# Optimization experiments

Measured on AMD Instinct MI355X. Metric: run time of the kernel, lower is better.

The kernel has to match this reference:

```python
import jax, jax.numpy as jnp
import numpy as np

N_HEAD = 16
N_EMBD = 1024
HEAD_DIM = N_EMBD // N_HEAD


def setup_inputs() -> dict:
    key = jax.random.key(0)
    k1, k2, k3 = jax.random.split(key, 3)
    B, T, C = 2, 2048, N_EMBD
    x = jax.random.normal(k1, (B, T, C), dtype=jnp.float32)
    # nn.Linear weights: (out_features, in_features)
    W_attn = jax.random.normal(k2, (3 * C, C), dtype=jnp.float32) * 0.02
    W_proj = jax.random.normal(k3, (C, C), dtype=jnp.float32) * 0.02
    return {"x": x, "W_attn": W_attn, "W_proj": W_proj}


def reference(x, W_attn, W_proj):
    B, T, C = x.shape
    h, hd = N_HEAD, HEAD_DIM
    # c_attn: x @ W^T, then split into q, k, v
    qkv = jnp.einsum('btc,dc->btd', x, W_attn)  # [B, T, 3C]
    q, k, v = jnp.split(qkv, 3, axis=-1)
    # [B, T, C] -> [B, h, T, hd]
    q = q.reshape(B, T, h, hd).transpose(0, 2, 1, 3)
    k = k.reshape(B, T, h, hd).transpose(0, 2, 1, 3)
    v = v.reshape(B, T, h, hd).transpose(0, 2, 1, 3)
    # NOTE: no 1/sqrt(hd) scaling in the original module
    logits = jnp.einsum('bhnk,bhmk->bhnm', q, k)  # [B, h, T, T]
    causal = jnp.tril(jnp.ones((T, T), dtype=bool))  # [T, T]
    logits = jnp.where(causal[None, None, :, :], logits, -jnp.inf)
    weights = jax.nn.softmax(logits, axis=-1)
    O = jnp.einsum('bhnm,bhmv->bhnv', weights, v)  # [B, h, T, hd]
    # Original: einsum('bhnv,hdv->bnd', O, c_proj.weight) with weight viewed as (h, d, v)
    Wp = W_proj.reshape(h, C, hd)
    Y = jnp.einsum('bhnv,hdv->bnd', O, Wp)  # [B, T, C]
    return Y
```

## Files before the change

### kernel.cpp

```cpp
#include <hip/hip_runtime.h>
#include <stdint.h>
#include <math.h>

#define B_    2
#define T_    2048
#define C_    1024
#define H_    16
#define D_    64
#define MTOT  4096
#define NQKV  3072
#define KDIM  1024

#define LOG2E 1.4426950408889634f

typedef short short8 __attribute__((ext_vector_type(8)));
typedef float f32x4  __attribute__((ext_vector_type(4)));

__device__ __forceinline__ uint16_t f2b(float f) {
    union { float f; uint32_t u; } x; x.f = f;
    uint32_t u = x.u;
    return (uint16_t)((u + 0x7FFFu + ((u >> 16) & 1u)) >> 16);
}
__device__ __forceinline__ uint32_t packb2(float a, float b) {
    union { float f; uint32_t u; } x, y; x.f = a; y.f = b;
    return __builtin_amdgcn_perm(y.u + 0x8000u, x.u + 0x8000u, 0x07060302u);
}
__device__ __forceinline__ uint32_t packb2_rne(float a, float b) {
    return (uint32_t)f2b(a) | ((uint32_t)f2b(b) << 16);
}
__device__ __forceinline__ float fexp2(float x) {
#if __has_builtin(__builtin_amdgcn_exp2f)
    return __builtin_amdgcn_exp2f(x);
#else
    return exp2f(x);
#endif
}

__global__ __launch_bounds__(256) void cast_all(const float* __restrict__ x,
                                                const float* __restrict__ wa,
                                                uint16_t* __restrict__ xb,
                                                uint16_t* __restrict__ wab,
                                                int n4x, int n4w) {
    int i = blockIdx.x * blockDim.x + threadIdx.x;
    const float* src; uint16_t* dst; int j;
    if (i < n4x) { src = x; dst = xb; j = i; }
    else { j = i - n4x; if (j >= n4w) return; src = wa; dst = wab; }
    float4 v = ((const float4*)src)[j];
    ushort4 o;
    o.x = f2b(v.x); o.y = f2b(v.y); o.z = f2b(v.z); o.w = f2b(v.w);
    ((ushort4*)dst)[j] = o;
}

__global__ __launch_bounds__(256) void cast_wp(const float* __restrict__ wp,
                                               uint16_t* __restrict__ wt) {
    int i = blockIdx.x * blockDim.x + threadIdx.x;
    int j4 = (i & 255) * 4;
    int d  = i >> 8;
    int h = j4 >> 6, v = j4 & 63;
    float4 val = *(const float4*)(wp + h * 65536 + d * 64 + v);
    ushort4 o;
    o.x = f2b(val.x); o.y = f2b(val.y); o.z = f2b(val.z); o.w = f2b(val.w);
    *(ushort4*)(wt + d * 1024 + j4) = o;
}

__global__ __launch_bounds__(256, 3) void gemm_qkv(const uint16_t* __restrict__ A,
                                                   const uint16_t* __restrict__ Bw,
                                                   uint16_t* __restrict__ qkvb) {
    __shared__ __align__(16) uint16_t As[128 * 64];
    __shared__ __align__(16) uint16_t Bs[128 * 64];

    int tid = threadIdx.x;
    int w = tid >> 6, lane = tid & 63;
    int qd = lane >> 4, ln = lane & 15;
    int lnx = ln & 7;
    int rowBase = blockIdx.y * 128;
    int colBase = blockIdx.x * 128;
    int mw = (w >> 1) * 64, nw = (w & 1) * 64;

    int srow = tid >> 3;
    int pchunk = tid & 7;
    int gchunk = pchunk ^ (srow & 7);

    const uint16_t* ga = A  + (size_t)(rowBase + srow) * KDIM + gchunk * 8;
    const uint16_t* gb = Bw + (size_t)(colBase + srow) * KDIM + gchunk * 8;
    uint16_t* la = &As[srow * 64 + pchunk * 8];
    uint16_t* lb = &Bs[srow * 64 + pchunk * 8];

    short8 pa[4], pb[4];
#pragma unroll
    for (int m = 0; m < 4; m++) {
        pa[m] = *(const short8*)(ga + (size_t)m * 32 * KDIM);
        pb[m] = *(const short8*)(gb + (size_t)m * 32 * KDIM);
    }

    f32x4 acc[4][4] = {};
    for (int s = 0; s < 16; s++) {
#pragma unroll
        for (int m = 0; m < 4; m++) {
            *(short8*)(la + m * 32 * 64) = pa[m];
            *(short8*)(lb + m * 32 * 64) = pb[m];
        }
        __syncthreads();
        if (s < 15) {
            int k0 = (s + 1) * 64;
#pragma unroll
            for (int m = 0; m < 4; m++) {
                pa[m] = *(const short8*)(ga + k0 + (size_t)m * 32 * KDIM);
                pb[m] = *(const short8*)(gb + k0 + (size_t)m * 32 * KDIM);
            }
        }
#pragma unroll
        for (int ks = 0; ks < 2; ks++) {
            int p = (ks * 4 + qd) ^ lnx;
            short8 a[4], b[4];
#pragma unroll
            for (int i = 0; i < 4; i++) {
                a[i] = *(const short8*)&As[(mw + i * 16 + ln) * 64 + p * 8];
                b[i] = *(const short8*)&Bs[(nw + i * 16 + ln) * 64 + p * 8];
            }
#pragma unroll
            for (int i = 0; i < 4; i++)
#pragma unroll
                for (int j = 0; j < 4; j++)
                    acc[i][j] = __builtin_amdgcn_mfma_f32_16x16x32_bf16(a[i], b[j], acc[i][j], 0, 0, 0);
        }
        __syncthreads();
    }

#pragma unroll
    for (int i = 0; i < 4; i++) {
#pragma unroll
        for (int j = 0; j < 4; j++) {
            int gcol = colBase + nw + j * 16 + ln;
            int which = gcol >> 10;
            int rem = gcol & 1023;
            int h = rem >> 6, d = rem & 63;
            float sc = (which == 0) ? LOG2E : 1.0f;
#pragma unroll
            for (int r = 0; r < 4; r++) {
                int grow = rowBase + mw + i * 16 + qd * 4 + r;
                int bb = grow >> 11, t = grow & 2047;
                uint16_t val = f2b(acc[i][j][r] * sc);
                if (which == 2) {
                    qkvb[(size_t)2 * 4194304 + (((size_t)(bb * H_ + h) * D_) + d) * T_ + t] = val;
                } else {
                    qkvb[(size_t)which * 4194304 + (((size_t)(bb * H_ + h) * T_) + t) * D_ + d] = val;
                }
            }
        }
    }
}

__global__ __launch_bounds__(256) void attn(const uint16_t* __restrict__ qkvb,
                                            uint16_t* __restrict__ oc) {
    union ShU {
        uint16_t Pl[4][64][72];
        f32x4 X[2][17][64];
    };
    __shared__ __align__(16) ShU sh;

    int tid = threadIdx.x;
    int w = tid >> 6, lane = tid & 63;
    int qd = lane >> 4, ln = lane & 15;
    int bid = blockIdx.x;
    int pr = bid >> 5;
    int bh = bid & 31;

    const uint16_t* Q  = qkvb + (size_t)bh * T_ * D_;
    const uint16_t* K  = Q + 4194304;
    const uint16_t* Vt = qkvb + (size_t)2 * 4194304 + (size_t)bh * D_ * T_;

    for (int phase = 0; phase < 2; phase++) {
        int qt = phase == 0 ? (31 - pr) : pr;
        int qbase = qt * 64;
        int ntiles = qt + 1;

        short8 bq[4][2];
#pragma unroll
        for (int jq = 0; jq < 4; jq++)
#pragma unroll
            for (int ks = 0; ks < 2; ks++)
                bq[jq][ks] = *(const short8*)(Q + (size_t)(qbase + jq * 16 + ln) * D_ + ks * 32 + qd * 8);

        f32x4 ot[4][4] = {};
        float l_part[4] = {};

        short8 ak[4][2];
        if (w < ntiles) {
#pragma unroll
            for (int it = 0; it < 4; it++)
#pragma unroll
                for (int ks = 0; ks < 2; ks++)
                    ak[it][ks] = *(const short8*)(K + (size_t)(w * 64 + it * 16 + ln) * D_ + ks * 32 + qd * 8);
        }

        for (int kt = w; kt < ntiles; kt += 4) {
            bool diag = (kt == qt);

#pragma unroll
            for (int it = 0; it < 2; it++) {
                f32x4 stt[4] = {};
#pragma unroll
                for (int ks = 0; ks < 2; ks++)
#pragma unroll
                    for (int jq = 0; jq < 4; jq++)
                        stt[jq] = __builtin_amdgcn_mfma_f32_16x16x32_bf16(ak[it][ks], bq[jq][ks], stt[jq], 0, 0, 0);
                if (diag) {
#pragma unroll
                    for (int jq = 0; jq < 4; jq++)
#pragma unroll
                        for (int r = 0; r < 4; r++) {
                            int t = it * 16 + qd * 4 + r;
                            int q = jq * 16 + ln;
                            if (t > q) stt[jq][r] = -1.0e30f;
                        }
                }
#pragma unroll
                for (int jq = 0; jq < 4; jq++) {
                    float p0 = fexp2(stt[jq][0]);
                    float p1 = fexp2(stt[jq][1]);
                    float p2 = fexp2(stt[jq][2]);
                    float p3 = fexp2(stt[jq][3]);
                    l_part[jq] += (p0 + p1) + (p2 + p3);
                    uint2 pk;
                    pk.x = packb2(p0, p1);
                    pk.y = packb2(p2, p3);
                    *(uint2*)&sh.Pl[w][jq * 16 + ln][it * 16 + qd * 4] = pk;
                }
            }

            short8 av[4][2];
#pragma unroll
            for (int id = 0; id < 4; id++)
#pragma unroll
                for (int ks = 0; ks < 2; ks++)
                    av[id][ks] = *(const short8*)(Vt + (size_t)(id * 16 + ln) * T_ + kt * 64 + ks * 32 + qd * 8);

            short8 bp0[4];
#pragma unroll
            for (int jq = 0; jq < 4; jq++)
                bp0[jq] = *(const short8*)&sh.Pl[w][jq * 16 + ln][qd * 8];

#pragma unroll
            for (int it = 2; it < 4; it++) {
                f32x4 stt[4] = {};
#pragma unroll
                for (int ks = 0; ks < 2; ks++)
#pragma unroll
                    for (int jq = 0; jq < 4; jq++)
                        stt[jq] = __builtin_amdgcn_mfma_f32_16x16x32_bf16(ak[it][ks], bq[jq][ks], stt[jq], 0, 0, 0);
                if (diag) {
#pragma unroll
                    for (int jq = 0; jq < 4; jq++)
#pragma unroll
                        for (int r = 0; r < 4; r++) {
                            int t = it * 16 + qd * 4 + r;
                            int q = jq * 16 + ln;
                            if (t > q) stt[jq][r] = -1.0e30f;
                        }
                }
#pragma unroll
                for (int jq = 0; jq < 4; jq++) {
                    float p0 = fexp2(stt[jq][0]);
                    float p1 = fexp2(stt[jq][1]);
                    float p2 = fexp2(stt[jq][2]);
                    float p3 = fexp2(stt[jq][3]);
                    l_part[jq] += (p0 + p1) + (p2 + p3);
                    uint2 pk;
                    pk.x = packb2(p0, p1);
                    pk.y = packb2(p2, p3);
                    *(uint2*)&sh.Pl[w][jq * 16 + ln][it * 16 + qd * 4] = pk;
                }
            }

            if (kt + 4 < ntiles) {
#pragma unroll
                for (int it = 0; it < 4; it++)
#pragma unroll
                    for (int ks = 0; ks < 2; ks++)
                        ak[it][ks] = *(const short8*)(K + (size_t)((kt + 4) * 64 + it * 16 + ln) * D_ + ks * 32 + qd * 8);
            }

            short8 bp1[4];
#pragma unroll
            for (int jq = 0; jq < 4; jq++)
                bp1[jq] = *(const short8*)&sh.Pl[w][jq * 16 + ln][32 + qd * 8];

#pragma unroll
            for (int id = 0; id < 4; id++)
#pragma unroll
                for (int jq = 0; jq < 4; jq++)
                    ot[id][jq] = __builtin_amdgcn_mfma_f32_16x16x32_bf16(av[id][0], bp0[jq], ot[id][jq], 0, 0, 0);
#pragma unroll
            for (int id = 0; id < 4; id++)
#pragma unroll
                for (int jq = 0; jq < 4; jq++)
                    ot[id][jq] = __builtin_amdgcn_mfma_f32_16x16x32_bf16(av[id][1], bp1[jq], ot[id][jq], 0, 0, 0);
        }

        f32x4 lp = { l_part[0], l_part[1], l_part[2], l_part[3] };
        __syncthreads();
        if (w >= 2) {
#pragma unroll
            for (int id = 0; id < 4; id++)
#pragma unroll
                for (int jq = 0; jq < 4; jq++)
                    sh.X[w - 2][id * 4 + jq][lane] = ot[id][jq];
            sh.X[w - 2][16][lane] = lp;
        }
        __syncthreads();
        if (w < 2) {
#pragma unroll
            for (int id = 0; id < 4; id++)
#pragma unroll
                for (int jq = 0; jq < 4; jq++)
                    ot[id][jq] += sh.X[w][id * 4 + jq][lane];
            lp += sh.X[w][16][lane];
        }
        __syncthreads();
        if (w == 1) {
#pragma unroll
            for (int id = 0; id < 4; id++)
#pragma unroll
                for (int jq = 0; jq < 4; jq++)
                    sh.X[0][id * 4 + jq][lane] = ot[id][jq];
            sh.X[0][16][lane] = lp;
        }
        __syncthreads();
        if (w == 0) {
#pragma unroll
            for (int id = 0; id < 4; id++)
#pragma unroll
                for (int jq = 0; jq < 4; jq++)
                    ot[id][jq] += sh.X[0][id * 4 + jq][lane];
            lp += sh.X[0][16][lane];
            float rl[4];
#pragma unroll
            for (int jq = 0; jq < 4; jq++) {
                float s = lp[jq];
                s += __shfl_xor(s, 16);
                s += __shfl_xor(s, 32);
                rl[jq] = 1.0f / s;
            }
            int b = bh >> 4, h = bh & 15;
#pragma unroll
            for (int id = 0; id < 4; id++)
#pragma unroll
                for (int jq = 0; jq < 4; jq++) {
                    float v0 = ot[id][jq][0] * rl[jq];
                    float v1 = ot[id][jq][1] * rl[jq];
                    float v2 = ot[id][jq][2] * rl[jq];
                    float v3 = ot[id][jq][3] * rl[jq];
                    uint2 pk;
                    pk.x = packb2_rne(v0, v1);
                    pk.y = packb2_rne(v2, v3);
                    int q = qbase + jq * 16 + ln;
                    *(uint2*)&oc[(size_t)(b * T_ + q) * C_ + h * 64 + id * 16 + qd * 4] = pk;
                }
        }
        __syncthreads();
    }
}

__global__ __launch_bounds__(256, 3) void gemm_out(const uint16_t* __restrict__ A,
                                                   const uint16_t* __restrict__ Bw,
                                                   float* __restrict__ out) {
    __shared__ __align__(16) uint16_t As[128 * 64];
    __shared__ __align__(16) uint16_t Bs[64 * 64];

    int tid = threadIdx.x;
    int w = tid >> 6, lane = tid & 63;
    int qd = lane >> 4, ln = lane & 15;
    int lnx = ln & 7;
    int rowBase = blockIdx.y * 128;
    int colBase = blockIdx.x * 64;
    int mw = (w >> 1) * 64, nw = (w & 1) * 32;

    int srow = tid >> 3;
    int pchunk = tid & 7;
    int gchunk = pchunk ^ (srow & 7);

    const uint16_t* ga = A  + (size_t)(rowBase + srow) * KDIM + gchunk * 8;
    const uint16_t* gb = Bw + (size_t)(colBase + srow) * KDIM + gchunk * 8;
    uint16_t* la = &As[srow * 64 + pchunk * 8];
    uint16_t* lb = &Bs[srow * 64 + pchunk * 8];

    short8 pa[4], pb[2];
#pragma unroll
    for (int m = 0; m < 4; m++)
        pa[m] = *(const short8*)(ga + (size_t)m * 32 * KDIM);
#pragma unroll
    for (int m = 0; m < 2; m++)
        pb[m] = *(const short8*)(gb + (size_t)m * 32 * KDIM);

    f32x4 acc[4][2] = {};
    for (int s = 0; s < 16; s++) {
#pragma unroll
        for (int m = 0; m < 4; m++)
            *(short8*)(la + m * 32 * 64) = pa[m];
#pragma unroll
        for (int m = 0; m < 2; m++)
            *(short8*)(lb + m * 32 * 64) = pb[m];
        __syncthreads();
        if (s < 15) {
            int k0 = (s + 1) * 64;
#pragma unroll
            for (int m = 0; m < 4; m++)
                pa[m] = *(const short8*)(ga + k0 + (size_t)m * 32 * KDIM);
#pragma unroll
            for (int m = 0; m < 2; m++)
                pb[m] = *(const short8*)(gb + k0 + (size_t)m * 32 * KDIM);
        }
#pragma unroll
        for (int ks = 0; ks < 2; ks++) {
            int p = (ks * 4 + qd) ^ lnx;
            short8 a[4], b[2];
#pragma unroll
            for (int i = 0; i < 4; i++)
                a[i] = *(const short8*)&As[(mw + i * 16 + ln) * 64 + p * 8];
#pragma unroll
            for (int j = 0; j < 2; j++)
                b[j] = *(const short8*)&Bs[(nw + j * 16 + ln) * 64 + p * 8];
#pragma unroll
            for (int i = 0; i < 4; i++)
#pragma unroll
                for (int j = 0; j < 2; j++)
                    acc[i][j] = __builtin_amdgcn_mfma_f32_16x16x32_bf16(a[i], b[j], acc[i][j], 0, 0, 0);
        }
        __syncthreads();
    }

#pragma unroll
    for (int i = 0; i < 4; i++)
#pragma unroll
        for (int j = 0; j < 2; j++)
#pragma unroll
            for (int r = 0; r < 4; r++) {
                int grow = rowBase + mw + i * 16 + qd * 4 + r;
                int gcol = colBase + nw + j * 16 + ln;
                out[(size_t)grow * 1024 + gcol] = acc[i][j][r];
            }
}

extern "C" void kernel_launch(void* const* d_in, const int* in_sizes, int n_in,
                              void* d_out, int out_size, void* d_ws, size_t ws_size,
                              hipStream_t stream) {
    const float* x  = (const float*)d_in[0];
    const float* Wa = (const float*)d_in[1];
    const float* Wp = (const float*)d_in[2];
    float* out = (float*)d_out;

    uint16_t* ws   = (uint16_t*)d_ws;
    uint16_t* xb   = ws;
    uint16_t* Wab  = xb + 4194304;
    uint16_t* Wtb  = Wab + 3145728;
    uint16_t* qkvb = Wtb + 1048576;
    uint16_t* ob   = qkvb + (size_t)3 * 4194304;

    cast_all<<<7168, 256, 0, stream>>>(x, Wa, xb, Wab, 4194304 / 4, 3145728 / 4);
    cast_wp<<<1024, 256, 0, stream>>>(Wp, Wtb);
    gemm_qkv<<<dim3(24, 32), 256, 0, stream>>>(xb, Wab, qkvb);
    attn<<<512, 256, 0, stream>>>(qkvb, ob);
    gemm_out<<<dim3(16, 32), 256, 0, stream>>>(ob, Wtb, out);
}
```

Before: 183.3 us.

## Fuse fp32-to-bf16 cast into QKV GEMM and halve attention query tile

The separate cast kernel for x and W_attn is dropped. The QKV GEMM now loads fp32 directly and converts to bf16 with round-to-nearest-even before writing to shared memory, which removes a full round trip of the inputs through global memory and one launch. The attention kernel's query tile shrinks from 64 to 32 rows, so the grid doubles to 1024 blocks and causal-triangle load balance improves. In exchange the GEMM reads twice the bytes per tile and does conversion work in its loop, and each attention block reloads K/V for fewer queries.

```diff
diff --git a/kernel.cpp b/kernel.cpp
--- a/kernel.cpp
+++ b/kernel.cpp
@@ -28,27 +28,20 @@
 __device__ __forceinline__ uint32_t packb2_rne(float a, float b) {
     return (uint32_t)f2b(a) | ((uint32_t)f2b(b) << 16);
 }
+__device__ __forceinline__ short8 cvt8(float4 a, float4 b) {
+    union { uint32_t u[4]; short8 s; } r;
+    r.u[0] = packb2_rne(a.x, a.y);
+    r.u[1] = packb2_rne(a.z, a.w);
+    r.u[2] = packb2_rne(b.x, b.y);
+    r.u[3] = packb2_rne(b.z, b.w);
+    return r.s;
+}
 __device__ __forceinline__ float fexp2(float x) {
 #if __has_builtin(__builtin_amdgcn_exp2f)
     return __builtin_amdgcn_exp2f(x);
 #else
     return exp2f(x);
 #endif
-}
-
-__global__ __launch_bounds__(256) void cast_all(const float* __restrict__ x,
-                                                const float* __restrict__ wa,
-                                                uint16_t* __restrict__ xb,
-                                                uint16_t* __restrict__ wab,
-                                                int n4x, int n4w) {
-    int i = blockIdx.x * blockDim.x + threadIdx.x;
-    const float* src; uint16_t* dst; int j;
-    if (i < n4x) { src = x; dst = xb; j = i; }
-    else { j = i - n4x; if (j >= n4w) return; src = wa; dst = wab; }
-    float4 v = ((const float4*)src)[j];
-    ushort4 o;
-    o.x = f2b(v.x); o.y = f2b(v.y); o.z = f2b(v.z); o.w = f2b(v.w);
-    ((ushort4*)dst)[j] = o;
 }
 
 __global__ __launch_bounds__(256) void cast_wp(const float* __restrict__ wp,
@@ -63,8 +56,8 @@
     *(ushort4*)(wt + d * 1024 + j4) = o;
 }
 
-__global__ __launch_bounds__(256, 3) void gemm_qkv(const uint16_t* __restrict__ A,
-                                                   const uint16_t* __restrict__ Bw,
+__global__ __launch_bounds__(256, 3) void gemm_qkv(const float* __restrict__ A,
+                                                   const float* __restrict__ Bw,
                                                    uint16_t* __restrict__ qkvb) {
     __shared__ __align__(16) uint16_t As[128 * 64];
     __shared__ __align__(16) uint16_t Bs[128 * 64];
@@ -81,32 +74,36 @@
     int pchunk = tid & 7;
     int gchunk = pchunk ^ (srow & 7);
 
-    const uint16_t* ga = A  + (size_t)(rowBase + srow) * KDIM + gchunk * 8;
-    const uint16_t* gb = Bw + (size_t)(colBase + srow) * KDIM + gchunk * 8;
+    const float* ga = A  + (size_t)(rowBase + srow) * KDIM + gchunk * 8;
+    const float* gb = Bw + (size_t)(colBase + srow) * KDIM + gchunk * 8;
     uint16_t* la = &As[srow * 64 + pchunk * 8];
     uint16_t* lb = &Bs[srow * 64 + pchunk * 8];
 
-    short8 pa[4], pb[4];
+    float4 pa[4][2], pb[4][2];
 #pragma unroll
     for (int m = 0; m < 4; m++) {
-        pa[m] = *(const short8*)(ga + (size_t)m * 32 * KDIM);
-        pb[m] = *(const short8*)(gb + (size_t)m * 32 * KDIM);
+        pa[m][0] = *(const float4*)(ga + (size_t)m * 32 * KDIM);
+        pa[m][1] = *(const float4*)(ga + (size_t)m * 32 * KDIM + 4);
+        pb[m][0] = *(const float4*)(gb + (size_t)m * 32 * KDIM);
+        pb[m][1] = *(const float4*)(gb + (size_t)m * 32 * KDIM + 4);
     }
 
     f32x4 acc[4][4] = {};
     for (int s = 0; s < 16; s++) {
 #pragma unroll
         for (int m = 0; m < 4; m++) {
-            *(short8*)(la + m * 32 * 64) = pa[m];
-            *(short8*)(lb + m * 32 * 64) = pb[m];
+            *(short8*)(la + m * 32 * 64) = cvt8(pa[m][0], pa[m][1]);
+            *(short8*)(lb + m * 32 * 64) = cvt8(pb[m][0], pb[m][1]);
         }
         __syncthreads();
         if (s < 15) {
             int k0 = (s + 1) * 64;
 #pragma unroll
             for (int m = 0; m < 4; m++) {
-                pa[m] = *(const short8*)(ga + k0 + (size_t)m * 32 * KDIM);
-                pb[m] = *(const short8*)(gb + k0 + (size_t)m * 32 * KDIM);
+                pa[m][0] = *(const float4*)(ga + k0 + (size_t)m * 32 * KDIM);
+                pa[m][1] = *(const float4*)(ga + k0 + (size_t)m * 32 * KDIM + 4);
+                pb[m][0] = *(const float4*)(gb + k0 + (size_t)m * 32 * KDIM);
+                pb[m][1] = *(const float4*)(gb + k0 + (size_t)m * 32 * KDIM + 4);
             }
         }
 #pragma unroll
@@ -154,8 +151,8 @@
 __global__ __launch_bounds__(256) void attn(const uint16_t* __restrict__ qkvb,
                                             uint16_t* __restrict__ oc) {
     union ShU {
-        uint16_t Pl[4][64][72];
-        f32x4 X[2][17][64];
+        uint16_t Pl[4][32][72];
+        f32x4 X[2][9][64];
     };
     __shared__ __align__(16) ShU sh;
 
@@ -171,19 +168,20 @@
     const uint16_t* Vt = qkvb + (size_t)2 * 4194304 + (size_t)bh * D_ * T_;
 
     for (int phase = 0; phase < 2; phase++) {
-        int qt = phase == 0 ? (31 - pr) : pr;
-        int qbase = qt * 64;
-        int ntiles = qt + 1;
-
-        short8 bq[4][2];
-#pragma unroll
-        for (int jq = 0; jq < 4; jq++)
+        int qt2 = phase == 0 ? (63 - pr) : pr;
+        int qbase = qt2 * 32;
+        int ntiles = (qt2 >> 1) + 1;
+        int dtile = qt2 >> 1;
+
+        short8 bq[2][2];
+#pragma unroll
+        for (int jq = 0; jq < 2; jq++)
 #pragma unroll
             for (int ks = 0; ks < 2; ks++)
                 bq[jq][ks] = *(const short8*)(Q + (size_t)(qbase + jq * 16 + ln) * D_ + ks * 32 + qd * 8);
 
-        f32x4 ot[4][4] = {};
-        float l_part[4] = {};
+        f32x4 ot[4][2] = {};
+        float l_part[2] = {};
 
         short8 ak[4][2];
         if (w < ntiles) {
@@ -195,28 +193,28 @@
         }
 
         for (int kt = w; kt < ntiles; kt += 4) {
-            bool diag = (kt == qt);
+            bool diag = (kt == dtile);
 
 #pragma unroll
             for (int it = 0; it < 2; it++) {
-                f32x4 stt[4] = {};
+                f32x4 stt[2] = {};
 #pragma unroll
                 for (int ks = 0; ks < 2; ks++)
 #pragma unroll
-                    for (int jq = 0; jq < 4; jq++)
+                    for (int jq = 0; jq < 2; jq++)
                         stt[jq] = __builtin_amdgcn_mfma_f32_16x16x32_bf16(ak[it][ks], bq[jq][ks], stt[jq], 0, 0, 0);
                 if (diag) {
 #pragma unroll
-                    for (int jq = 0; jq < 4; jq++)
+                    for (int jq = 0; jq < 2; jq++)
 #pragma unroll
                         for (int r = 0; r < 4; r++) {
-                            int t = it * 16 + qd * 4 + r;
-                            int q = jq * 16 + ln;
+                            int t = kt * 64 + it * 16 + qd * 4 + r;
+                            int q = qbase + jq * 16 + ln;
                             if (t > q) stt[jq][r] = -1.0e30f;
                         }
                 }
 #pragma unroll
-                for (int jq = 0; jq < 4; jq++) {
+                for (int jq = 0; jq < 2; jq++) {
                     float p0 = fexp2(stt[jq][0]);
                     float p1 = fexp2(stt[jq][1]);
                     float p2 = fexp2(stt[jq][2]);
@@ -236,31 +234,31 @@
                 for (int ks = 0; ks < 2; ks++)
                     av[id][ks] = *(const short8*)(Vt + (size_t)(id * 16 + ln) * T_ + kt * 64 + ks * 32 + qd * 8);
 
-            short8 bp0[4];
-#pragma unroll
-            for (int jq = 0; jq < 4; jq++)
+            short8 bp0[2];
+#pragma unroll
+            for (int jq = 0; jq < 2; jq++)
                 bp0[jq] = *(const short8*)&sh.Pl[w][jq * 16 + ln][qd * 8];
 
 #pragma unroll
             for (int it = 2; it < 4; it++) {
-                f32x4 stt[4] = {};
+                f32x4 stt[2] = {};
 #pragma unroll
                 for (int ks = 0; ks < 2; ks++)
 #pragma unroll
-                    for (int jq = 0; jq < 4; jq++)
+                    for (int jq = 0; jq < 2; jq++)
                         stt[jq] = __builtin_amdgcn_mfma_f32_16x16x32_bf16(ak[it][ks], bq[jq][ks], stt[jq], 0, 0, 0);
                 if (diag) {
 #pragma unroll
-                    for (int jq = 0; jq < 4; jq++)
+                    for (int jq = 0; jq < 2; jq++)
 #pragma unroll
                         for (int r = 0; r < 4; r++) {
-                            int t = it * 16 + qd * 4 + r;
-                            int q = jq * 16 + ln;
+                            int t = kt * 64 + it * 16 + qd * 4 + r;
+                            int q = qbase + jq * 16 + ln;
                             if (t > q) stt[jq][r] = -1.0e30f;
                         }
                 }
 #pragma unroll
-                for (int jq = 0; jq < 4; jq++) {
+                for (int jq = 0; jq < 2; jq++) {
                     float p0 = fexp2(stt[jq][0]);
                     float p1 = fexp2(stt[jq][1]);
                     float p2 = fexp2(stt[jq][2]);
@@ -281,62 +279,62 @@
                         ak[it][ks] = *(const short8*)(K + (size_t)((kt + 4) * 64 + it * 16 + ln) * D_ + ks * 32 + qd * 8);
             }
 
-            short8 bp1[4];
-#pragma unroll
-            for (int jq = 0; jq < 4; jq++)
+            short8 bp1[2];
+#pragma unroll
+            for (int jq = 0; jq < 2; jq++)
                 bp1[jq] = *(const short8*)&sh.Pl[w][jq * 16 + ln][32 + qd * 8];
 
 #pragma unroll
             for (int id = 0; id < 4; id++)
 #pragma unroll
-                for (int jq = 0; jq < 4; jq++)
+                for (int jq = 0; jq < 2; jq++)
                     ot[id][jq] = __builtin_amdgcn_mfma_f32_16x16x32_bf16(av[id][0], bp0[jq], ot[id][jq], 0, 0, 0);
 #pragma unroll
             for (int id = 0; id < 4; id++)
 #pragma unroll
-                for (int jq = 0; jq < 4; jq++)
+                for (int jq = 0; jq < 2; jq++)
                     ot[id][jq] = __builtin_amdgcn_mfma_f32_16x16x32_bf16(av[id][1], bp1[jq], ot[id][jq], 0, 0, 0);
         }
 
-        f32x4 lp = { l_part[0], l_part[1], l_part[2], l_part[3] };
+        f32x4 lp = { l_part[0], l_part[1], 0.f, 0.f };
         __syncthreads();
         if (w >= 2) {
 #pragma unroll
             for (int id = 0; id < 4; id++)
 #pragma unroll
-                for (int jq = 0; jq < 4; jq++)
-                    sh.X[w - 2][id * 4 + jq][lane] = ot[id][jq];
-            sh.X[w - 2][16][lane] = lp;
+                for (int jq = 0; jq < 2; jq++)
+                    sh.X[w - 2][id * 2 + jq][lane] = ot[id][jq];
+            sh.X[w - 2][8][lane] = lp;
         }
         __syncthreads();
         if (w < 2) {
 #pragma unroll
             for (int id = 0; id < 4; id++)
 #pragma unroll
-                for (int jq = 0; jq < 4; jq++)
-                    ot[id][jq] += sh.X[w][id * 4 + jq][lane];
-            lp += sh.X[w][16][lane];
+                for (int jq = 0; jq < 2; jq++)
+                    ot[id][jq] += sh.X[w][id * 2 + jq][lane];
+            lp += sh.X[w][8][lane];
         }
         __syncthreads();
         if (w == 1) {
 #pragma unroll
             for (int id = 0; id < 4; id++)
 #pragma unroll
-                for (int jq = 0; jq < 4; jq++)
-                    sh.X[0][id * 4 + jq][lane] = ot[id][jq];
-            sh.X[0][16][lane] = lp;
+                for (int jq = 0; jq < 2; jq++)
+                    sh.X[0][id * 2 + jq][lane] = ot[id][jq];
+            sh.X[0][8][lane] = lp;
         }
         __syncthreads();
         if (w == 0) {
 #pragma unroll
             for (int id = 0; id < 4; id++)
 #pragma unroll
-                for (int jq = 0; jq < 4; jq++)
-                    ot[id][jq] += sh.X[0][id * 4 + jq][lane];
-            lp += sh.X[0][16][lane];
-            float rl[4];
-#pragma unroll
-            for (int jq = 0; jq < 4; jq++) {
+                for (int jq = 0; jq < 2; jq++)
+                    ot[id][jq] += sh.X[0][id * 2 + jq][lane];
+            lp += sh.X[0][8][lane];
+            float rl[2];
+#pragma unroll
+            for (int jq = 0; jq < 2; jq++) {
                 float s = lp[jq];
                 s += __shfl_xor(s, 16);
                 s += __shfl_xor(s, 32);
@@ -346,7 +344,7 @@
 #pragma unroll
             for (int id = 0; id < 4; id++)
 #pragma unroll
-                for (int jq = 0; jq < 4; jq++) {
+                for (int jq = 0; jq < 2; jq++) {
                     float v0 = ot[id][jq][0] * rl[jq];
                     float v1 = ot[id][jq][1] * rl[jq];
                     float v2 = ot[id][jq][2] * rl[jq];
@@ -451,15 +449,12 @@
     float* out = (float*)d_out;
 
     uint16_t* ws   = (uint16_t*)d_ws;
-    uint16_t* xb   = ws;
-    uint16_t* Wab  = xb + 4194304;
-    uint16_t* Wtb  = Wab + 3145728;
+    uint16_t* Wtb  = ws;
     uint16_t* qkvb = Wtb + 1048576;
     uint16_t* ob   = qkvb + (size_t)3 * 4194304;
 
-    cast_all<<<7168, 256, 0, stream>>>(x, Wa, xb, Wab, 4194304 / 4, 3145728 / 4);
     cast_wp<<<1024, 256, 0, stream>>>(Wp, Wtb);
-    gemm_qkv<<<dim3(24, 32), 256, 0, stream>>>(xb, Wab, qkvb);
-    attn<<<512, 256, 0, stream>>>(qkvb, ob);
+    gemm_qkv<<<dim3(24, 32), 256, 0, stream>>>(x, Wa, qkvb);
+    attn<<<1024, 256, 0, stream>>>(qkvb, ob);
     gemm_out<<<dim3(16, 32), 256, 0, stream>>>(ob, Wtb, out);
 }
```

Result: slower. 215.5 us (+17.5%).
